# Kernel optimization log

Hardware: AMD Instinct MI355X
Metric: run time of the kernel (lower is better)

Reference implementation:

```python
import jax, jax.numpy as jnp
import numpy as np

DIM = 128

def _layernorm(x, g, b, eps=1e-5):
    mu = jnp.mean(x, axis=-1, keepdims=True)
    var = jnp.var(x, axis=-1, keepdims=True)
    return (x - mu) * jax.lax.rsqrt(var + eps) * g + b

def setup_inputs() -> dict:
    key = jax.random.key(0)
    ks = jax.random.split(key, 12)
    B, T, O, d = 64, 1024, 128, DIM
    s = 1.0 / np.sqrt(d)
    s2 = 1.0 / np.sqrt(2 * d)
    return {
        "token_nodes": jax.random.normal(ks[0], (B, T, d), jnp.float32),
        "obj_nodes": jax.random.normal(ks[1], (B, O, d), jnp.float32),
        "attn_to_obj": jax.random.uniform(ks[2], (B, T, O), jnp.float32),
        "W_msg_o": jax.random.uniform(ks[3], (d, d), jnp.float32, -s, s),
        "b_msg_o": jnp.zeros((d,), jnp.float32),
        "W_msg_t": jax.random.uniform(ks[4], (d, d), jnp.float32, -s, s),
        "b_msg_t": jnp.zeros((d,), jnp.float32),
        "W_upd_t": jax.random.uniform(ks[5], (2 * d, d), jnp.float32, -s2, s2),
        "b_upd_t": jnp.zeros((d,), jnp.float32),
        "W_upd_o": jax.random.uniform(ks[6], (2 * d, d), jnp.float32, -s2, s2),
        "b_upd_o": jnp.zeros((d,), jnp.float32),
        "g_ln_t": jnp.ones((d,), jnp.float32),
        "beta_ln_t": jnp.zeros((d,), jnp.float32),
        "g_ln_o": jnp.ones((d,), jnp.float32),
        "beta_ln_o": jnp.zeros((d,), jnp.float32),
    }

def reference(token_nodes, obj_nodes, attn_to_obj,
              W_msg_o, b_msg_o, W_msg_t, b_msg_t,
              W_upd_t, b_upd_t, W_upd_o, b_upd_o,
              g_ln_t, beta_ln_t, g_ln_o, beta_ln_o):
    # messages from objects -> tokens
    msg_o = obj_nodes @ W_msg_o + b_msg_o                      # [B,O,d]
    agg_to_t = jnp.einsum('bto,bod->btd', attn_to_obj, msg_o)  # [B,T,d]
    # messages from tokens -> objects (transposed attention)
    msg_t = token_nodes @ W_msg_t + b_msg_t                    # [B,T,d]
    agg_to_o = jnp.einsum('bto,btd->bod', attn_to_obj, msg_t)  # [B,O,d]
    # fused update MLPs (dropout is identity in eval mode)
    new_t = jax.nn.relu(jnp.concatenate([token_nodes, agg_to_t], axis=-1) @ W_upd_t + b_upd_t)
    new_o = jax.nn.relu(jnp.concatenate([obj_nodes, agg_to_o], axis=-1) @ W_upd_o + b_upd_o)
    new_t = _layernorm(token_nodes + new_t, g_ln_t, beta_ln_t)
    new_o = _layernorm(obj_nodes + new_o, g_ln_o, beta_ln_o)
    return (new_t, new_o)
```

## Files before the change

kernel.cpp:

```cpp
#include <hip/hip_runtime.h>

typedef unsigned short u16;
typedef __attribute__((ext_vector_type(8))) short bf16x8;
typedef __attribute__((ext_vector_type(4))) float f32x4;

#define NB 64
#define NT 1024
#define NO 128
#define ND 128

__device__ __forceinline__ u16 f2bf(float f) {
    union { float f; unsigned u; } v; v.f = f;
    unsigned r = v.u + 0x7FFFu + ((v.u >> 16) & 1u);
    return (u16)(r >> 16);
}
__device__ __forceinline__ float bf2f(short s) {
    union { unsigned u; float f; } v; v.u = ((unsigned)(u16)s) << 16; return v.f;
}

__device__ __forceinline__ bf16x8 frag_from_f32(const float* p) {
    const float4 a = *reinterpret_cast<const float4*>(p);
    const float4 b = *reinterpret_cast<const float4*>(p + 4);
    bf16x8 r;
    r[0] = (short)f2bf(a.x); r[1] = (short)f2bf(a.y);
    r[2] = (short)f2bf(a.z); r[3] = (short)f2bf(a.w);
    r[4] = (short)f2bf(b.x); r[5] = (short)f2bf(b.y);
    r[6] = (short)f2bf(b.z); r[7] = (short)f2bf(b.w);
    return r;
}

__global__ __launch_bounds__(256, 4)
void k_msg_o(const float* __restrict__ obj, const float* __restrict__ Wmo,
             const float* __restrict__ bmo,
             const float* __restrict__ Wmt, const float* __restrict__ Wut,
             const float* __restrict__ Wuo,
             u16* __restrict__ msg_oT, u16* __restrict__ WmtT,
             u16* __restrict__ WutT, u16* __restrict__ WuoT) {
    __shared__ u16 wT[128][136];
    __shared__ u16 lds_m[128][72];
    int bid = blockIdx.x;
    int tid = threadIdx.x;

    for (int idx = bid * 256 + tid; idx < 81920; idx += 32768) {
        if (idx < 16384) {
            int k = idx >> 7, n = idx & 127;
            WmtT[n * 128 + k] = f2bf(Wmt[idx]);
        } else if (idx < 49152) {
            int i2 = idx - 16384; int k = i2 >> 7, n = i2 & 127;
            WutT[n * 256 + (k ^ ((n & 7) << 3))] = f2bf(Wut[i2]);
        } else {
            int i2 = idx - 49152; int k = i2 >> 7, n = i2 & 127;
            WuoT[n * 256 + k] = f2bf(Wuo[i2]);
        }
    }
#pragma unroll
    for (int i = 0; i < 64; i++) {
        int idx = i * 256 + tid;
        int k = idx >> 7, n = idx & 127;
        wT[n][k] = f2bf(Wmo[idx]);
    }
    __syncthreads();

    int rows_base = bid * 64;
    int l = tid & 63, w = tid >> 6;
    int l15 = l & 15, lk = (l >> 4) * 8, rsub = (l >> 4) * 4;
    int wrow = w * 16;
    int row0 = rows_base + wrow;

    f32x4 acc[8] = {};
    const float* xp = obj + (size_t)(row0 + l15) * 128;
#pragma unroll
    for (int kk = 0; kk < 4; kk++) {
        bf16x8 a = frag_from_f32(xp + kk * 32 + lk);
#pragma unroll
        for (int ct = 0; ct < 8; ct++) {
            bf16x8 bfr = *reinterpret_cast<const bf16x8*>(&wT[ct * 16 + l15][kk * 32 + lk]);
            acc[ct] = __builtin_amdgcn_mfma_f32_16x16x32_bf16(a, bfr, acc[ct], 0, 0, 0);
        }
    }
#pragma unroll
    for (int ct = 0; ct < 8; ct++) {
        int n = ct * 16 + l15;
        float bv = bmo[n];
        ushort4 pk;
        pk.x = f2bf(acc[ct][0] + bv);
        pk.y = f2bf(acc[ct][1] + bv);
        pk.z = f2bf(acc[ct][2] + bv);
        pk.w = f2bf(acc[ct][3] + bv);
        *reinterpret_cast<ushort4*>(&lds_m[n][wrow + rsub]) = pk;
    }
    __syncthreads();
    int n = tid >> 1, h = tid & 1;
    const u16* src = &lds_m[n][h * 32];
    int b = rows_base >> 7, o0 = rows_base & 127;
    u16* rowp = msg_oT + (size_t)(b * 128 + n) * 128;
#pragma unroll
    for (int i = 0; i < 4; i++) {
        int off = o0 + h * 32 + i * 8;
        *reinterpret_cast<bf16x8*>(rowp + (off ^ ((n & 7) << 3))) =
            *reinterpret_cast<const bf16x8*>(src + i * 8);
    }
}

__global__ __launch_bounds__(512, 4)
void k_P(const float* __restrict__ attn, const float* __restrict__ tok,
         u16* __restrict__ Psl, float* __restrict__ rs_part) {
    __shared__ u16 aT[128 * 128];
    __shared__ u16 dT[128 * 128];
    int b = blockIdx.x >> 2, ks = blockIdx.x & 3;
    int tid = threadIdx.x;
    int l = tid & 63, w = tid >> 6;
    int l15 = l & 15, lk = (l >> 4) * 8, rsub = (l >> 4) * 4;
    int ro = w * 16 + l15;
    int og = (tid & 31) * 4;
    int tg = tid >> 5;

    f32x4 acc[8] = {};
    float rsum = 0.f;
#pragma unroll
    for (int c = 0; c < 2; c++) {
        int kb = ks * 256 + c * 128;
        const float* asrc = attn + ((size_t)b * NT + kb) * 128;
        const float* tsrc = tok  + ((size_t)b * NT + kb) * 128;
        if (c) __syncthreads();
#pragma unroll
        for (int half = 0; half < 2; half++) {
            const float* src = half ? tsrc : asrc;
            u16* buf = half ? dT : aT;
            int t0 = tg * 8;
            f32x4 v[8];
#pragma unroll
            for (int i = 0; i < 8; i++)
                v[i] = *reinterpret_cast<const f32x4*>(src + (size_t)(t0 + i) * 128 + og);
            int gr = t0 >> 3;
#pragma unroll
            for (int j = 0; j < 4; j++) {
                int o = og + j;
                bf16x8 pk;
#pragma unroll
                for (int i = 0; i < 8; i++) pk[i] = (short)f2bf(v[i][j]);
                *reinterpret_cast<bf16x8*>(&buf[o * 128 + ((gr ^ (o & 15)) << 3)]) = pk;
            }
        }
        __syncthreads();
#pragma unroll
        for (int kk = 0; kk < 4; kk++) {
            int tt = kk * 32 + lk;
            bf16x8 a = *reinterpret_cast<const bf16x8*>(
                &aT[ro * 128 + (((tt >> 3) ^ (ro & 15)) << 3)]);
#pragma unroll
            for (int i = 0; i < 8; i++) rsum += bf2f(a[i]);
#pragma unroll
            for (int ct = 0; ct < 8; ct++) {
                int d = ct * 16 + l15;
                bf16x8 bf = *reinterpret_cast<const bf16x8*>(
                    &dT[d * 128 + (((tt >> 3) ^ (d & 15)) << 3)]);
                acc[ct] = __builtin_amdgcn_mfma_f32_16x16x32_bf16(a, bf, acc[ct], 0, 0, 0);
            }
        }
    }
    rsum += __shfl_xor(rsum, 16, 64);
    rsum += __shfl_xor(rsum, 32, 64);
    if (l < 16) rs_part[((size_t)ks * NB + b) * NO + w * 16 + l15] = rsum;
    u16* pout = Psl + (((size_t)(ks * NB + b)) * NO + w * 16) * ND;
#pragma unroll
    for (int ct = 0; ct < 8; ct++)
#pragma unroll
        for (int r = 0; r < 4; r++)
            pout[(size_t)(rsub + r) * ND + ct * 16 + l15] = f2bf(acc[ct][r]);
}

__global__ __launch_bounds__(256, 4)
void k_obj_final(const float* __restrict__ obj, const u16* __restrict__ Psl,
                 const float* __restrict__ rs_part, const u16* __restrict__ WmtT,
                 const float* __restrict__ bmt, const u16* __restrict__ WuoT,
                 const float* __restrict__ buo, const float* __restrict__ g,
                 const float* __restrict__ beta, float* __restrict__ out) {
    __shared__ u16 P_lds[32][136];
    __shared__ u16 agg_lds[32][136];
    __shared__ float rs_lds[32];
    __shared__ float part_s[32][2], part_sq[32][2];
    int bid = blockIdx.x;
    int b = bid >> 2, ot = bid & 3;
    int ob = ot * 32;
    int tid = threadIdx.x;
    {
        int row = tid >> 3, c0 = (tid & 7) * 16;
        float sm[16];
#pragma unroll
        for (int i = 0; i < 16; i++) sm[i] = 0.f;
#pragma unroll
        for (int ks = 0; ks < 4; ks++) {
            const u16* p = Psl + (((size_t)(ks * NB + b)) * NO + ob + row) * ND + c0;
            bf16x8 v0 = *reinterpret_cast<const bf16x8*>(p);
            bf16x8 v1 = *reinterpret_cast<const bf16x8*>(p + 8);
#pragma unroll
            for (int i = 0; i < 8; i++) { sm[i] += bf2f(v0[i]); sm[8 + i] += bf2f(v1[i]); }
        }
#pragma unroll
        for (int j = 0; j < 4; j++) {
            ushort4 pk;
            pk.x = f2bf(sm[j * 4 + 0]); pk.y = f2bf(sm[j * 4 + 1]);
            pk.z = f2bf(sm[j * 4 + 2]); pk.w = f2bf(sm[j * 4 + 3]);
            *reinterpret_cast<ushort4*>(&P_lds[row][c0 + j * 4]) = pk;
        }
        if (tid < 32) {
            float r = 0.f;
#pragma unroll
            for (int ks = 0; ks < 4; ks++) r += rs_part[((size_t)ks * NB + b) * NO + ob + tid];
            rs_lds[tid] = r;
        }
    }
    __syncthreads();
    int l = tid & 63, w = tid >> 6;
    int l15 = l & 15, lk = (l >> 4) * 8, rsub = (l >> 4) * 4;
    int wr = (w & 1) * 16, wc = (w >> 1) * 64;
    f32x4 agg[4] = {};
#pragma unroll
    for (int kk = 0; kk < 4; kk++) {
        bf16x8 a = *reinterpret_cast<const bf16x8*>(&P_lds[wr + l15][kk * 32 + lk]);
#pragma unroll
        for (int ct = 0; ct < 4; ct++) {
            bf16x8 bf = *reinterpret_cast<const bf16x8*>(WmtT + (wc + ct * 16 + l15) * 128 + kk * 32 + lk);
            agg[ct] = __builtin_amdgcn_mfma_f32_16x16x32_bf16(a, bf, agg[ct], 0, 0, 0);
        }
    }
#pragma unroll
    for (int ct = 0; ct < 4; ct++) {
        int n = wc + ct * 16 + l15;
        float bb = bmt[n];
#pragma unroll
        for (int r = 0; r < 4; r++) {
            float v = agg[ct][r] + rs_lds[wr + rsub + r] * bb;
            agg_lds[wr + rsub + r][n] = f2bf(v);
        }
    }
    __syncthreads();
    f32x4 accm[4] = {};
    const float* objp = obj + ((size_t)(b * NO) + ob + wr + l15) * ND;
#pragma unroll
    for (int kk = 0; kk < 8; kk++) {
        int k0 = kk * 32;
        bf16x8 a = (k0 < 128) ? frag_from_f32(objp + k0 + lk)
                              : *reinterpret_cast<const bf16x8*>(&agg_lds[wr + l15][k0 - 128 + lk]);
#pragma unroll
        for (int ct = 0; ct < 4; ct++) {
            bf16x8 bf = *reinterpret_cast<const bf16x8*>(WuoT + (wc + ct * 16 + l15) * 256 + k0 + lk);
            accm[ct] = __builtin_amdgcn_mfma_f32_16x16x32_bf16(a, bf, accm[ct], 0, 0, 0);
        }
    }
    const float* objr = obj + ((size_t)(b * NO) + ob) * ND;
    float s[4] = {0.f, 0.f, 0.f, 0.f}, sq[4] = {0.f, 0.f, 0.f, 0.f};
#pragma unroll
    for (int ct = 0; ct < 4; ct++) {
        int n = wc + ct * 16 + l15;
        float bv = buo[n];
#pragma unroll
        for (int r = 0; r < 4; r++) {
            int lr = wr + rsub + r;
            float v = objr[(size_t)lr * ND + n] + fmaxf(accm[ct][r] + bv, 0.f);
            accm[ct][r] = v;
            s[r] += v;
            sq[r] += v * v;
        }
    }
#pragma unroll
    for (int ofs = 1; ofs < 16; ofs <<= 1) {
#pragma unroll
        for (int r = 0; r < 4; r++) {
            s[r]  += __shfl_xor(s[r], ofs, 64);
            sq[r] += __shfl_xor(sq[r], ofs, 64);
        }
    }
    if (l15 < 4) {
        float sv = (l15 == 0) ? s[0] : (l15 == 1) ? s[1] : (l15 == 2) ? s[2] : s[3];
        float qv = (l15 == 0) ? sq[0] : (l15 == 1) ? sq[1] : (l15 == 2) ? sq[2] : sq[3];
        part_s[wr + rsub + l15][w >> 1] = sv;
        part_sq[wr + rsub + l15][w >> 1] = qv;
    }
    __syncthreads();
    float mu[4], rstd[4];
#pragma unroll
    for (int r = 0; r < 4; r++) {
        int lr = wr + rsub + r;
        float st = part_s[lr][0] + part_s[lr][1];
        float qt = part_sq[lr][0] + part_sq[lr][1];
        mu[r] = st * (1.f / 128.f);
        rstd[r] = rsqrtf(qt * (1.f / 128.f) - mu[r] * mu[r] + 1e-5f);
    }
#pragma unroll
    for (int ct = 0; ct < 4; ct++) {
        int n = wc + ct * 16 + l15;
        float gn = g[n], bn = beta[n];
#pragma unroll
        for (int r = 0; r < 4; r++) {
            int lr = wr + rsub + r;
            out[((size_t)(b * NO) + ob + lr) * ND + n] = (accm[ct][r] - mu[r]) * rstd[r] * gn + bn;
        }
    }
}

__global__ __launch_bounds__(512, 2)
void k_token_update(const float* __restrict__ tok, const float* __restrict__ attn,
                    const u16* __restrict__ msg_oT, const u16* __restrict__ WutT,
                    const float* __restrict__ bupd, const float* __restrict__ g,
                    const float* __restrict__ beta, float* __restrict__ out) {
    __shared__ u16 msg_lds[16384];
    __shared__ u16 wut_lds[32768];
    __shared__ u16 agg_b[8][16][136];
    int b = blockIdx.x >> 2, bq = blockIdx.x & 3;
    int tid = threadIdx.x;
    {
        const u16* msrc = msg_oT + (size_t)b * 16384;
#pragma unroll
        for (int i = 0; i < 4; i++) {
            int idx = (i * 512 + tid) * 8;
            *reinterpret_cast<bf16x8*>(&msg_lds[idx]) = *reinterpret_cast<const bf16x8*>(msrc + idx);
        }
#pragma unroll
        for (int i = 0; i < 8; i++) {
            int idx = (i * 512 + tid) * 8;
            *reinterpret_cast<bf16x8*>(&wut_lds[idx]) = *reinterpret_cast<const bf16x8*>(WutT + idx);
        }
    }
    __syncthreads();
    int l = tid & 63, w = tid >> 6;
    int l15 = l & 15, lk = (l >> 4) * 8, rsub = (l >> 4) * 4;

#pragma unroll
    for (int pass = 0; pass < 2; pass++) {
        int trow = bq * 256 + pass * 128 + w * 16;
        size_t rbase = (size_t)b * NT + trow;

        const float* aF = attn + (rbase + l15) * NO;
        bf16x8 af[4];
#pragma unroll
        for (int kk = 0; kk < 4; kk++)
            af[kk] = frag_from_f32(aF + kk * 32 + lk);
        f32x4 acc[8] = {};
#pragma unroll
        for (int kk = 0; kk < 4; kk++) {
#pragma unroll
            for (int ct = 0; ct < 8; ct++) {
                int n = ct * 16 + l15;
                bf16x8 bf = *reinterpret_cast<const bf16x8*>(
                    &msg_lds[n * 128 + ((kk * 32 + lk) ^ ((n & 7) << 3))]);
                acc[ct] = __builtin_amdgcn_mfma_f32_16x16x32_bf16(af[kk], bf, acc[ct], 0, 0, 0);
            }
        }
#pragma unroll
        for (int ct = 0; ct < 8; ct++) {
            int n = ct * 16 + l15;
#pragma unroll
            for (int r = 0; r < 4; r++)
                agg_b[w][rsub + r][n] = f2bf(acc[ct][r]);
        }
        asm volatile("s_waitcnt lgkmcnt(0)" ::: "memory");
        __builtin_amdgcn_sched_barrier(0);
        const float* tokp = tok + (rbase + l15) * ND;
        bf16x8 am[8];
#pragma unroll
        for (int kk = 0; kk < 4; kk++)
            am[kk] = frag_from_f32(tokp + kk * 32 + lk);
#pragma unroll
        for (int kk = 0; kk < 4; kk++)
            am[4 + kk] = *reinterpret_cast<const bf16x8*>(&agg_b[w][l15][kk * 32 + lk]);
        f32x4 accm[8] = {};
#pragma unroll
        for (int kk = 0; kk < 8; kk++) {
#pragma unroll
            for (int ct = 0; ct < 8; ct++) {
                int n = ct * 16 + l15;
                bf16x8 bf = *reinterpret_cast<const bf16x8*>(
                    &wut_lds[n * 256 + ((kk * 32 + lk) ^ ((n & 7) << 3))]);
                accm[ct] = __builtin_amdgcn_mfma_f32_16x16x32_bf16(am[kk], bf, accm[ct], 0, 0, 0);
            }
        }
        const float* tokr = tok + rbase * ND;
        float s[4] = {0.f, 0.f, 0.f, 0.f}, sq[4] = {0.f, 0.f, 0.f, 0.f};
#pragma unroll
        for (int ct = 0; ct < 8; ct++) {
            int n = ct * 16 + l15;
            float bv = bupd[n];
#pragma unroll
            for (int r = 0; r < 4; r++) {
                float v = tokr[(size_t)(rsub + r) * ND + n] + fmaxf(accm[ct][r] + bv, 0.f);
                accm[ct][r] = v;
                s[r] += v;
                sq[r] += v * v;
            }
        }
#pragma unroll
        for (int ofs = 1; ofs < 16; ofs <<= 1) {
#pragma unroll
            for (int r = 0; r < 4; r++) {
                s[r]  += __shfl_xor(s[r], ofs, 64);
                sq[r] += __shfl_xor(sq[r], ofs, 64);
            }
        }
        float mu[4], rstd[4];
#pragma unroll
        for (int r = 0; r < 4; r++) {
            mu[r] = s[r] * (1.f / 128.f);
            rstd[r] = rsqrtf(sq[r] * (1.f / 128.f) - mu[r] * mu[r] + 1e-5f);
        }
#pragma unroll
        for (int ct = 0; ct < 8; ct++) {
            int n = ct * 16 + l15;
            float gn = g[n], bn = beta[n];
#pragma unroll
            for (int r = 0; r < 4; r++)
                out[(rbase + rsub + r) * ND + n] = (accm[ct][r] - mu[r]) * rstd[r] * gn + bn;
        }
    }
}

extern "C" void kernel_launch(void* const* d_in, const int* in_sizes, int n_in,
                              void* d_out, int out_size, void* d_ws, size_t ws_size,
                              hipStream_t stream) {
    const float* tok  = (const float*)d_in[0];
    const float* obj  = (const float*)d_in[1];
    const float* attn = (const float*)d_in[2];
    const float* Wmo  = (const float*)d_in[3];
    const float* bmo  = (const float*)d_in[4];
    const float* Wmt  = (const float*)d_in[5];
    const float* bmt  = (const float*)d_in[6];
    const float* Wut  = (const float*)d_in[7];
    const float* but  = (const float*)d_in[8];
    const float* Wuo  = (const float*)d_in[9];
    const float* buo  = (const float*)d_in[10];
    const float* gt   = (const float*)d_in[11];
    const float* bt   = (const float*)d_in[12];
    const float* go   = (const float*)d_in[13];
    const float* bo   = (const float*)d_in[14];
    float* out = (float*)d_out;

    u16* ws = (u16*)d_ws;
    u16* msg_oT = ws;
    u16* WmtT   = msg_oT + 1048576;
    u16* WutT   = WmtT + 16384;
    u16* WuoT   = WutT + 32768;
    u16* Psl    = WuoT + 32768;
    float* rs_part = (float*)(Psl + 4194304);

    k_msg_o<<<dim3(128), dim3(256), 0, stream>>>(obj, Wmo, bmo, Wmt, Wut, Wuo,
                                                 msg_oT, WmtT, WutT, WuoT);
    k_P<<<dim3(256), dim3(512), 0, stream>>>(attn, tok, Psl, rs_part);
    k_token_update<<<dim3(256), dim3(512), 0, stream>>>(tok, attn, msg_oT, WutT, but, gt, bt, out);
    k_obj_final<<<dim3(256), dim3(256), 0, stream>>>(obj, Psl, rs_part, WmtT, bmt, WuoT, buo, go, bo,
                                                     out + (size_t)NB * NT * ND);
}
```

Measured before the change: 61.44 us.

## Fuse msg_o projection and weight conversion into k_P, remap token_update blocks

Removes the separate k_msg_o launch by folding the weight bf16 conversion into every k_P block and the obj@W_msg_o projection into the ks==0 blocks, which reuse LDS after the P computation. k_token_update gets a block index remap that groups batches across consecutive blocks, likely for cache locality. It also hoists the token fragment and residual loads ahead of the first MFMA stage so their latency overlaps with compute. The trade-off is extra tail work on a quarter of the k_P blocks and higher register pressure from holding the residuals.

```diff
diff --git a/kernel.cpp b/kernel.cpp
--- a/kernel.cpp
+++ b/kernel.cpp
@@ -29,86 +29,33 @@
     return r;
 }
 
-__global__ __launch_bounds__(256, 4)
-void k_msg_o(const float* __restrict__ obj, const float* __restrict__ Wmo,
-             const float* __restrict__ bmo,
-             const float* __restrict__ Wmt, const float* __restrict__ Wut,
-             const float* __restrict__ Wuo,
-             u16* __restrict__ msg_oT, u16* __restrict__ WmtT,
-             u16* __restrict__ WutT, u16* __restrict__ WuoT) {
-    __shared__ u16 wT[128][136];
-    __shared__ u16 lds_m[128][72];
-    int bid = blockIdx.x;
+__global__ __launch_bounds__(512, 4)
+void k_P(const float* __restrict__ attn, const float* __restrict__ tok,
+         const float* __restrict__ obj, const float* __restrict__ Wmo,
+         const float* __restrict__ bmo, const float* __restrict__ Wmt,
+         const float* __restrict__ Wut, const float* __restrict__ Wuo,
+         u16* __restrict__ Psl, float* __restrict__ rs_part,
+         u16* __restrict__ msg_oT, u16* __restrict__ WmtT,
+         u16* __restrict__ WutT, u16* __restrict__ WuoT) {
+    __shared__ u16 aT[128 * 128];
+    __shared__ u16 dT[128 * 128];
+    int b = blockIdx.x >> 2, ks = blockIdx.x & 3;
     int tid = threadIdx.x;
 
-    for (int idx = bid * 256 + tid; idx < 81920; idx += 32768) {
+    {
+        int idx = blockIdx.x * 512 + tid;
         if (idx < 16384) {
             int k = idx >> 7, n = idx & 127;
             WmtT[n * 128 + k] = f2bf(Wmt[idx]);
         } else if (idx < 49152) {
             int i2 = idx - 16384; int k = i2 >> 7, n = i2 & 127;
             WutT[n * 256 + (k ^ ((n & 7) << 3))] = f2bf(Wut[i2]);
-        } else {
+        } else if (idx < 81920) {
             int i2 = idx - 49152; int k = i2 >> 7, n = i2 & 127;
             WuoT[n * 256 + k] = f2bf(Wuo[i2]);
         }
     }
-#pragma unroll
-    for (int i = 0; i < 64; i++) {
-        int idx = i * 256 + tid;
-        int k = idx >> 7, n = idx & 127;
-        wT[n][k] = f2bf(Wmo[idx]);
-    }
-    __syncthreads();
-
-    int rows_base = bid * 64;
-    int l = tid & 63, w = tid >> 6;
-    int l15 = l & 15, lk = (l >> 4) * 8, rsub = (l >> 4) * 4;
-    int wrow = w * 16;
-    int row0 = rows_base + wrow;
-
-    f32x4 acc[8] = {};
-    const float* xp = obj + (size_t)(row0 + l15) * 128;
-#pragma unroll
-    for (int kk = 0; kk < 4; kk++) {
-        bf16x8 a = frag_from_f32(xp + kk * 32 + lk);
-#pragma unroll
-        for (int ct = 0; ct < 8; ct++) {
-            bf16x8 bfr = *reinterpret_cast<const bf16x8*>(&wT[ct * 16 + l15][kk * 32 + lk]);
-            acc[ct] = __builtin_amdgcn_mfma_f32_16x16x32_bf16(a, bfr, acc[ct], 0, 0, 0);
-        }
-    }
-#pragma unroll
-    for (int ct = 0; ct < 8; ct++) {
-        int n = ct * 16 + l15;
-        float bv = bmo[n];
-        ushort4 pk;
-        pk.x = f2bf(acc[ct][0] + bv);
-        pk.y = f2bf(acc[ct][1] + bv);
-        pk.z = f2bf(acc[ct][2] + bv);
-        pk.w = f2bf(acc[ct][3] + bv);
-        *reinterpret_cast<ushort4*>(&lds_m[n][wrow + rsub]) = pk;
-    }
-    __syncthreads();
-    int n = tid >> 1, h = tid & 1;
-    const u16* src = &lds_m[n][h * 32];
-    int b = rows_base >> 7, o0 = rows_base & 127;
-    u16* rowp = msg_oT + (size_t)(b * 128 + n) * 128;
-#pragma unroll
-    for (int i = 0; i < 4; i++) {
-        int off = o0 + h * 32 + i * 8;
-        *reinterpret_cast<bf16x8*>(rowp + (off ^ ((n & 7) << 3))) =
-            *reinterpret_cast<const bf16x8*>(src + i * 8);
-    }
-}
-
-__global__ __launch_bounds__(512, 4)
-void k_P(const float* __restrict__ attn, const float* __restrict__ tok,
-         u16* __restrict__ Psl, float* __restrict__ rs_part) {
-    __shared__ u16 aT[128 * 128];
-    __shared__ u16 dT[128 * 128];
-    int b = blockIdx.x >> 2, ks = blockIdx.x & 3;
-    int tid = threadIdx.x;
+
     int l = tid & 63, w = tid >> 6;
     int l15 = l & 15, lk = (l >> 4) * 8, rsub = (l >> 4) * 4;
     int ro = w * 16 + l15;
@@ -168,6 +115,49 @@
 #pragma unroll
         for (int r = 0; r < 4; r++)
             pout[(size_t)(rsub + r) * ND + ct * 16 + l15] = f2bf(acc[ct][r]);
+
+    if (ks == 0) {
+        __syncthreads();
+#pragma unroll
+        for (int i = 0; i < 32; i++) {
+            int idx = i * 512 + tid;
+            int k = idx >> 7, n = idx & 127;
+            aT[n * 128 + (k ^ ((n & 7) << 3))] = f2bf(Wmo[idx]);
+        }
+        __syncthreads();
+        f32x4 mc[8] = {};
+        const float* xp = obj + ((size_t)b * NO + w * 16 + l15) * 128;
+#pragma unroll
+        for (int kk = 0; kk < 4; kk++) {
+            bf16x8 a = frag_from_f32(xp + kk * 32 + lk);
+#pragma unroll
+            for (int ct = 0; ct < 8; ct++) {
+                int n = ct * 16 + l15;
+                bf16x8 bfr = *reinterpret_cast<const bf16x8*>(
+                    &aT[n * 128 + ((kk * 32 + lk) ^ ((n & 7) << 3))]);
+                mc[ct] = __builtin_amdgcn_mfma_f32_16x16x32_bf16(a, bfr, mc[ct], 0, 0, 0);
+            }
+        }
+#pragma unroll
+        for (int ct = 0; ct < 8; ct++) {
+            int n = ct * 16 + l15;
+            float bv = bmo[n];
+            ushort4 pk;
+            pk.x = f2bf(mc[ct][0] + bv);
+            pk.y = f2bf(mc[ct][1] + bv);
+            pk.z = f2bf(mc[ct][2] + bv);
+            pk.w = f2bf(mc[ct][3] + bv);
+            int o = w * 16 + rsub;
+            *reinterpret_cast<ushort4*>(&dT[n * 128 + (o ^ ((n & 7) << 3))]) = pk;
+        }
+        __syncthreads();
+        u16* mout = msg_oT + (size_t)b * 16384;
+#pragma unroll
+        for (int i = 0; i < 4; i++) {
+            int idx2 = (i * 512 + tid) * 8;
+            *reinterpret_cast<bf16x8*>(mout + idx2) = *reinterpret_cast<const bf16x8*>(&dT[idx2]);
+        }
+    }
 }
 
 __global__ __launch_bounds__(256, 4)
@@ -308,18 +298,20 @@
     __shared__ u16 msg_lds[16384];
     __shared__ u16 wut_lds[32768];
     __shared__ u16 agg_b[8][16][136];
-    int b = blockIdx.x >> 2, bq = blockIdx.x & 3;
+    int i = blockIdx.x;
+    int b  = ((i >> 5) << 3) + (i & 7);
+    int bq = (i >> 3) & 3;
     int tid = threadIdx.x;
     {
         const u16* msrc = msg_oT + (size_t)b * 16384;
 #pragma unroll
-        for (int i = 0; i < 4; i++) {
-            int idx = (i * 512 + tid) * 8;
+        for (int k = 0; k < 4; k++) {
+            int idx = (k * 512 + tid) * 8;
             *reinterpret_cast<bf16x8*>(&msg_lds[idx]) = *reinterpret_cast<const bf16x8*>(msrc + idx);
         }
 #pragma unroll
-        for (int i = 0; i < 8; i++) {
-            int idx = (i * 512 + tid) * 8;
+        for (int k = 0; k < 8; k++) {
+            int idx = (k * 512 + tid) * 8;
             *reinterpret_cast<bf16x8*>(&wut_lds[idx]) = *reinterpret_cast<const bf16x8*>(WutT + idx);
         }
     }
@@ -331,12 +323,25 @@
     for (int pass = 0; pass < 2; pass++) {
         int trow = bq * 256 + pass * 128 + w * 16;
         size_t rbase = (size_t)b * NT + trow;
-
-        const float* aF = attn + (rbase + l15) * NO;
+        const float* aF   = attn + (rbase + l15) * NO;
+        const float* tokp = tok + (rbase + l15) * ND;
+        const float* tokr = tok + rbase * ND;
+
         bf16x8 af[4];
 #pragma unroll
         for (int kk = 0; kk < 4; kk++)
             af[kk] = frag_from_f32(aF + kk * 32 + lk);
+        bf16x8 am0[4];
+#pragma unroll
+        for (int kk = 0; kk < 4; kk++)
+            am0[kk] = frag_from_f32(tokp + kk * 32 + lk);
+        float resv[8][4];
+#pragma unroll
+        for (int ct = 0; ct < 8; ct++)
+#pragma unroll
+            for (int r = 0; r < 4; r++)
+                resv[ct][r] = tokr[(size_t)(rsub + r) * ND + ct * 16 + l15];
+
         f32x4 acc[8] = {};
 #pragma unroll
         for (int kk = 0; kk < 4; kk++) {
@@ -357,11 +362,9 @@
         }
         asm volatile("s_waitcnt lgkmcnt(0)" ::: "memory");
         __builtin_amdgcn_sched_barrier(0);
-        const float* tokp = tok + (rbase + l15) * ND;
         bf16x8 am[8];
 #pragma unroll
-        for (int kk = 0; kk < 4; kk++)
-            am[kk] = frag_from_f32(tokp + kk * 32 + lk);
+        for (int kk = 0; kk < 4; kk++) am[kk] = am0[kk];
 #pragma unroll
         for (int kk = 0; kk < 4; kk++)
             am[4 + kk] = *reinterpret_cast<const bf16x8*>(&agg_b[w][l15][kk * 32 + lk]);
@@ -376,7 +379,6 @@
                 accm[ct] = __builtin_amdgcn_mfma_f32_16x16x32_bf16(am[kk], bf, accm[ct], 0, 0, 0);
             }
         }
-        const float* tokr = tok + rbase * ND;
         float s[4] = {0.f, 0.f, 0.f, 0.f}, sq[4] = {0.f, 0.f, 0.f, 0.f};
 #pragma unroll
         for (int ct = 0; ct < 8; ct++) {
@@ -384,7 +386,7 @@
             float bv = bupd[n];
 #pragma unroll
             for (int r = 0; r < 4; r++) {
-                float v = tokr[(size_t)(rsub + r) * ND + n] + fmaxf(accm[ct][r] + bv, 0.f);
+                float v = resv[ct][r] + fmaxf(accm[ct][r] + bv, 0.f);
                 accm[ct][r] = v;
                 s[r] += v;
                 sq[r] += v * v;
@@ -443,9 +445,8 @@
     u16* Psl    = WuoT + 32768;
     float* rs_part = (float*)(Psl + 4194304);
 
-    k_msg_o<<<dim3(128), dim3(256), 0, stream>>>(obj, Wmo, bmo, Wmt, Wut, Wuo,
-                                                 msg_oT, WmtT, WutT, WuoT);
-    k_P<<<dim3(256), dim3(512), 0, stream>>>(attn, tok, Psl, rs_part);
+    k_P<<<dim3(256), dim3(512), 0, stream>>>(attn, tok, obj, Wmo, bmo, Wmt, Wut, Wuo,
+                                             Psl, rs_part, msg_oT, WmtT, WutT, WuoT);
     k_token_update<<<dim3(256), dim3(512), 0, stream>>>(tok, attn, msg_oT, WutT, but, gt, bt, out);
     k_obj_final<<<dim3(256), dim3(256), 0, stream>>>(obj, Psl, rs_part, WmtT, bmt, WuoT, buo, go, bo,
                                                      out + (size_t)NB * NT * ND);
```

New measurement: 55.70 us (median of 2 runs). 1.1x faster.
